# Performance work log

Hardware: AMD Instinct MI355X
Metric: run time of the kernel (lower is better)

Reference implementation:

```python
import jax, jax.numpy as jnp
import numpy as np

B, N, D_IN, D_H, D_OUT = 2, 512, 128, 128, 128


def _mlp2(x, W1, b1, W2, b2):
    # Linear -> SiLU -> Linear
    h = jax.nn.silu(x @ W1 + b1)
    return h @ W2 + b2


def _safe_norm(d2):
    # norm with zero (not NaN) gradient at 0, matching torch.norm's subgradient
    pos = d2 > 0
    return jnp.where(pos, jnp.sqrt(jnp.where(pos, d2, 1.0)), 0.0)


def setup_inputs() -> dict:
    key = jax.random.key(0)
    ks = jax.random.split(key, 16)

    def lin(k, fan_in, fan_out):
        bound = 1.0 / np.sqrt(fan_in)
        kw, kb = jax.random.split(k)
        W = jax.random.uniform(kw, (fan_in, fan_out), jnp.float32, -bound, bound)
        b = jax.random.uniform(kb, (fan_out,), jnp.float32, -bound, bound)
        return W, b

    Ws1, bs1 = lin(ks[0], D_IN, D_H)
    Ws2, bs2 = lin(ks[1], D_H, D_OUT)
    Wv1, bv1 = lin(ks[2], D_IN, D_H)
    Wv2, bv2 = lin(ks[3], D_H, D_OUT)
    Wa1, ba1 = lin(ks[4], D_IN + 3, D_H)
    Wa2, ba2 = lin(ks[5], D_H, 1)

    node_features = jax.random.normal(ks[6], (B, N, D_IN), jnp.float32)
    coordinates = jax.random.normal(ks[7], (B, N, 3), jnp.float32)
    edge_mask = jax.random.randint(ks[8], (B, N, N), 0, 2, jnp.int32)

    return dict(node_features=node_features, coordinates=coordinates, edge_mask=edge_mask,
                Ws1=Ws1, bs1=bs1, Ws2=Ws2, bs2=bs2,
                Wv1=Wv1, bv1=bv1, Wv2=Wv2, bv2=bv2,
                Wa1=Wa1, ba1=ba1, Wa2=Wa2, ba2=ba2)


def reference(node_features, coordinates, edge_mask,
              Ws1, bs1, Ws2, bs2, Wv1, bv1, Wv2, bv2, Wa1, ba1, Wa2, ba2):
    num_atoms = node_features.shape[1]

    # pairwise geometry: diff[b,i,j,:] = x_i - x_j
    diff = coordinates[:, :, None, :] - coordinates[:, None, :, :]  # [B,N,N,3]
    d2 = jnp.sum(diff * diff, axis=-1)
    distances = _safe_norm(d2)  # [B,N,N]

    # per-node scalar branch
    scalar_features = _mlp2(node_features, Ws1, bs1, Ws2, bs2)  # [B,N,D_OUT]

    # radial features + broadcast node features -> attention MLP
    dist_features = jnp.stack(
        [distances, 1.0 / (distances + 1e-6), jnp.exp(-distances)], axis=-1)  # [B,N,N,3]
    nf_exp = jnp.broadcast_to(node_features[:, :, None, :],
                              node_features.shape[:2] + (num_atoms, node_features.shape[-1]))
    attention_input = jnp.concatenate([nf_exp, dist_features], axis=-1)  # [B,N,N,D_IN+3]
    attn_logits = _mlp2(attention_input, Wa1, ba1, Wa2, ba2)[..., 0]  # [B,N,N]

    attn_logits = jnp.where(edge_mask != 0, attn_logits, -jnp.inf)
    attention_weights = jax.nn.softmax(attn_logits, axis=-1)  # [B,N,N]

    # direction-weighted aggregation
    vector_aggregated = jnp.einsum('bijc,bij->bic', diff, attention_weights)  # [B,N,3]

    vector_features = _mlp2(node_features, Wv1, bv1, Wv2, bv2)  # [B,N,D_OUT]
    vector_out = vector_aggregated * vector_features[..., :3]  # [B,N,3]

    return scalar_features, vector_out
```

## Files before the change

### kernel.cpp

```cpp
#include <hip/hip_runtime.h>
#include <math.h>

#define NB 2
#define NN 512
#define DD 128
#define LOG2E 1.4426950408889634f

typedef unsigned long long ull;

__device__ __forceinline__ float exp2_hw(float x) {
    float r; asm("v_exp_f32 %0, %1" : "=v"(r) : "v"(x)); return r;
}
__device__ __forceinline__ float silu_f(float x) {
    float e = exp2_hw(-LOG2E * x);
    return x * __builtin_amdgcn_rcpf(1.0f + e);
}

__global__ __launch_bounds__(256) void k_all(
    const float* __restrict__ nf,
    const float* __restrict__ coords,
    const int*   __restrict__ mask,
    const float* __restrict__ Ws1, const float* __restrict__ bs1,
    const float* __restrict__ Ws2, const float* __restrict__ bs2,
    const float* __restrict__ Wv1, const float* __restrict__ bv1,
    const float* __restrict__ Wv2, const float* __restrict__ bv2,
    const float* __restrict__ Wa1, const float* __restrict__ ba1,
    const float* __restrict__ Wa2, const float* __restrict__ ba2p,
    float* __restrict__ scalar_out,
    float* __restrict__ vec_out)
{
    __shared__ float  s_nf[DD];
    __shared__ float  s_part[3][256];
    __shared__ float  s_hs[DD];
    __shared__ float  s_hv[DD];
    __shared__ float4 s_pk[DD];
    __shared__ float  s_am[DD];
    __shared__ short  s_act[NN];
    __shared__ int    s_cnt8[8], s_off8[8], s_nactS;
    __shared__ float  s_red[4], s_red2[4][4];

    const int row  = blockIdx.x;
    const int b    = row >> 9;
    const int tid  = threadIdx.x;
    const int lane = tid & 63;
    const int wid  = tid >> 6;
    const int c    = tid & 127;
    const int h    = tid >> 7;

    if (tid < DD) s_nf[tid] = nf[row * DD + tid];
    __syncthreads();

    {
        float ps = 0.f, pv = 0.f, pa = 0.f;
        const int k0 = h * 64;
        #pragma unroll 8
        for (int kk = 0; kk < 64; ++kk) {
            int k   = k0 + kk;
            float x = s_nf[k];
            ps = fmaf(x, Ws1[k * DD + c], ps);
            pv = fmaf(x, Wv1[k * DD + c], pv);
            pa = fmaf(x, Wa1[k * DD + c], pa);
        }
        s_part[0][tid] = ps;
        s_part[1][tid] = pv;
        s_part[2][tid] = pa;
    }
    const int* mrow = mask + (size_t)row * NN;
    const bool m0 = (mrow[tid]       != 0);
    const bool m1 = (mrow[tid + 256] != 0);
    const ull  bal0 = __ballot(m0);
    const ull  bal1 = __ballot(m1);
    if (lane == 0) {
        s_cnt8[wid]     = __popcll(bal0);
        s_cnt8[4 + wid] = __popcll(bal1);
    }
    __syncthreads();

    if (tid < DD) {
        s_hs[tid] = silu_f(s_part[0][tid] + s_part[0][128 + tid] + bs1[tid]);
        s_hv[tid] = silu_f(s_part[1][tid] + s_part[1][128 + tid] + bv1[tid]);
        float base = s_part[2][tid] + s_part[2][128 + tid] + ba1[tid];
        float4 p;
        p.x = -LOG2E * base;
        p.y = -LOG2E * Wa1[128 * DD + tid];
        p.z = -LOG2E * Wa1[129 * DD + tid];
        p.w = -LOG2E * Wa1[130 * DD + tid];
        s_pk[tid] = p;
        s_am[tid] = -Wa2[tid];
    }
    if (tid == 0) {
        int acc = 0;
        #pragma unroll
        for (int q = 0; q < 8; ++q) { s_off8[q] = acc; acc += s_cnt8[q]; }
        s_nactS = acc;
    }
    __syncthreads();

    {
        float pb = 0.f;
        const int k0 = h * 64;
        #pragma unroll 8
        for (int kk = 0; kk < 64; ++kk) {
            int k = k0 + kk;
            pb = fmaf(s_hs[k], Ws2[k * DD + c], pb);
        }
        s_part[0][tid] = pb;
    }
    if (tid >= 128 && tid < 224) {
        int idx = tid - 128;
        int col = idx >> 5;
        int kq  = idx & 31;
        float vp = 0.f;
        #pragma unroll
        for (int u = 0; u < 4; ++u) {
            int k = 4 * kq + u;
            vp = fmaf(s_hv[k], Wv2[k * DD + col], vp);
        }
        s_part[1][tid] = vp;
    }
    {
        const ull lmask = (1ull << lane) - 1ull;
        if (m0) s_act[s_off8[wid]     + __popcll(bal0 & lmask)] = (short)tid;
        if (m1) s_act[s_off8[4 + wid] + __popcll(bal1 & lmask)] = (short)(tid + 256);
    }
    __syncthreads();

    if (tid < DD) {
        scalar_out[row * DD + tid] = s_part[0][tid] + s_part[0][128 + tid] + bs2[tid];
    }
    float vf_col = 0.f;
    if (tid < 3) {
        float v = bv2[tid];
        const float* pp = &s_part[1][128 + tid * 32];
        for (int r = 0; r < 32; ++r) v += pp[r];
        vf_col = v;
    }
    const int nact = s_nactS;

    const float ba2l = ba2p[0] * LOG2E;
    const float xi0 = coords[row * 3 + 0];
    const float xi1 = coords[row * 3 + 1];
    const float xi2 = coords[row * 3 + 2];
    const float* cb = coords + (size_t)b * NN * 3;
    const float4* A4 = (const float4*)s_am;

    float lg0 = 0.f, dx0 = 0.f, dy0 = 0.f, dz0 = 0.f;
    float lg1 = 0.f, dx1 = 0.f, dy1 = 0.f, dz1 = 0.f;
    const bool act0 = (tid < nact);
    const bool act1 = (tid + 256 < nact);

    if (act0) {
        int j = (int)s_act[tid];
        dx0 = xi0 - cb[j * 3 + 0];
        dy0 = xi1 - cb[j * 3 + 1];
        dz0 = xi2 - cb[j * 3 + 2];
        float d2 = fmaf(dx0, dx0, fmaf(dy0, dy0, dz0 * dz0));
        float d  = sqrtf(d2);
        float f1 = d;
        float x  = d + 1e-6f;
        float rc = __builtin_amdgcn_rcpf(x);
        float f2 = rc * fmaf(-x, rc, 2.0f);
        float f3 = exp2_hw(-LOG2E * d);
        float acc = ba2l;
        for (int t4 = 0; t4 < DD / 4; ++t4) {
            float4 A = A4[t4];
            { float4 P = s_pk[4*t4+0]; float pre = fmaf(f3,P.w,fmaf(f2,P.z,fmaf(f1,P.y,P.x)));
              float e = exp2_hw(pre); float r = __builtin_amdgcn_rcpf(1.0f+e);
              acc = fmaf(pre*A.x, r, acc); }
            { float4 P = s_pk[4*t4+1]; float pre = fmaf(f3,P.w,fmaf(f2,P.z,fmaf(f1,P.y,P.x)));
              float e = exp2_hw(pre); float r = __builtin_amdgcn_rcpf(1.0f+e);
              acc = fmaf(pre*A.y, r, acc); }
            { float4 P = s_pk[4*t4+2]; float pre = fmaf(f3,P.w,fmaf(f2,P.z,fmaf(f1,P.y,P.x)));
              float e = exp2_hw(pre); float r = __builtin_amdgcn_rcpf(1.0f+e);
              acc = fmaf(pre*A.z, r, acc); }
            { float4 P = s_pk[4*t4+3]; float pre = fmaf(f3,P.w,fmaf(f2,P.z,fmaf(f1,P.y,P.x)));
              float e = exp2_hw(pre); float r = __builtin_amdgcn_rcpf(1.0f+e);
              acc = fmaf(pre*A.w, r, acc); }
        }
        lg0 = acc;
    }
    if (act1) {
        int j = (int)s_act[tid + 256];
        dx1 = xi0 - cb[j * 3 + 0];
        dy1 = xi1 - cb[j * 3 + 1];
        dz1 = xi2 - cb[j * 3 + 2];
        float d2 = fmaf(dx1, dx1, fmaf(dy1, dy1, dz1 * dz1));
        float d  = sqrtf(d2);
        float f1 = d;
        float x  = d + 1e-6f;
        float rc = __builtin_amdgcn_rcpf(x);
        float f2 = rc * fmaf(-x, rc, 2.0f);
        float f3 = exp2_hw(-LOG2E * d);
        float acc = ba2l;
        for (int t4 = 0; t4 < DD / 4; ++t4) {
            float4 A = A4[t4];
            { float4 P = s_pk[4*t4+0]; float pre = fmaf(f3,P.w,fmaf(f2,P.z,fmaf(f1,P.y,P.x)));
              float e = exp2_hw(pre); float r = __builtin_amdgcn_rcpf(1.0f+e);
              acc = fmaf(pre*A.x, r, acc); }
            { float4 P = s_pk[4*t4+1]; float pre = fmaf(f3,P.w,fmaf(f2,P.z,fmaf(f1,P.y,P.x)));
              float e = exp2_hw(pre); float r = __builtin_amdgcn_rcpf(1.0f+e);
              acc = fmaf(pre*A.y, r, acc); }
            { float4 P = s_pk[4*t4+2]; float pre = fmaf(f3,P.w,fmaf(f2,P.z,fmaf(f1,P.y,P.x)));
              float e = exp2_hw(pre); float r = __builtin_amdgcn_rcpf(1.0f+e);
              acc = fmaf(pre*A.z, r, acc); }
            { float4 P = s_pk[4*t4+3]; float pre = fmaf(f3,P.w,fmaf(f2,P.z,fmaf(f1,P.y,P.x)));
              float e = exp2_hw(pre); float r = __builtin_amdgcn_rcpf(1.0f+e);
              acc = fmaf(pre*A.w, r, acc); }
        }
        lg1 = acc;
    }

    float mloc = -__builtin_inff();
    if (act0) mloc = lg0;
    if (act1) mloc = fmaxf(mloc, lg1);
    #pragma unroll
    for (int ofs = 32; ofs >= 1; ofs >>= 1) mloc = fmaxf(mloc, __shfl_xor(mloc, ofs));
    if (lane == 0) s_red[wid] = mloc;
    __syncthreads();
    const float mx = fmaxf(fmaxf(s_red[0], s_red[1]), fmaxf(s_red[2], s_red[3]));

    float es = 0.f, wx = 0.f, wy = 0.f, wz = 0.f;
    if (act0) {
        float e = exp2_hw(lg0 - mx);
        es += e; wx = fmaf(e, dx0, wx); wy = fmaf(e, dy0, wy); wz = fmaf(e, dz0, wz);
    }
    if (act1) {
        float e = exp2_hw(lg1 - mx);
        es += e; wx = fmaf(e, dx1, wx); wy = fmaf(e, dy1, wy); wz = fmaf(e, dz1, wz);
    }
    #pragma unroll
    for (int ofs = 32; ofs >= 1; ofs >>= 1) {
        es += __shfl_xor(es, ofs);
        wx += __shfl_xor(wx, ofs);
        wy += __shfl_xor(wy, ofs);
        wz += __shfl_xor(wz, ofs);
    }
    if (lane == 0) {
        s_red2[wid][0] = es; s_red2[wid][1] = wx;
        s_red2[wid][2] = wy; s_red2[wid][3] = wz;
    }
    __syncthreads();

    if (tid < 3) {
        float tot = s_red2[0][0] + s_red2[1][0] + s_red2[2][0] + s_red2[3][0];
        float num = s_red2[0][1+tid] + s_red2[1][1+tid] + s_red2[2][1+tid] + s_red2[3][1+tid];
        vec_out[row * 3 + tid] = (num / tot) * vf_col;
    }
}

extern "C" void kernel_launch(void* const* d_in, const int* in_sizes, int n_in,
                              void* d_out, int out_size, void* d_ws, size_t ws_size,
                              hipStream_t stream) {
    const float* nf     = (const float*)d_in[0];
    const float* coords = (const float*)d_in[1];
    const int*   mask   = (const int*)  d_in[2];
    const float* Ws1 = (const float*)d_in[3];  const float* bs1 = (const float*)d_in[4];
    const float* Ws2 = (const float*)d_in[5];  const float* bs2 = (const float*)d_in[6];
    const float* Wv1 = (const float*)d_in[7];  const float* bv1 = (const float*)d_in[8];
    const float* Wv2 = (const float*)d_in[9];  const float* bv2 = (const float*)d_in[10];
    const float* Wa1 = (const float*)d_in[11]; const float* ba1 = (const float*)d_in[12];
    const float* Wa2 = (const float*)d_in[13]; const float* ba2 = (const float*)d_in[14];

    float* scalar_out = (float*)d_out;
    float* vec_out    = (float*)d_out + NB * NN * DD;

    hipLaunchKernelGGL(k_all, dim3(NB * NN), dim3(256), 0, stream,
                       nf, coords, mask,
                       Ws1, bs1, Ws2, bs2, Wv1, bv1, Wv2, bv2,
                       Wa1, ba1, Wa2, ba2,
                       scalar_out, vec_out);
}
```

Before: 28.49 us.

## Overlap attention logit loop with second-layer GEMV and merge per-edge loops

Moves the attention-logit computation ahead of the barrier so it runs alongside the second-layer matvecs. It also fuses the two per-edge loops into one loop that shares the LDS loads of the packed weights, and makes the second slot wave-uniform so only partially active waves compute it. The first-layer and second-layer matvecs now read node features as float4, and the active-count prefix scan is moved earlier. The risks are extra register pressure from keeping two edge states live at once, and idle lanes in partially active waves doing wasted work.

Result: faster. 27.83 us (-2.3%).

```diff
diff --git a/kernel.cpp b/kernel.cpp
--- a/kernel.cpp
+++ b/kernel.cpp
@@ -15,6 +15,12 @@
     float e = exp2_hw(-LOG2E * x);
     return x * __builtin_amdgcn_rcpf(1.0f + e);
 }
+
+#define UPD(P, Ae, ff1, ff2, ff3, accv)                                       \
+    { float pre = fmaf(ff3, P.w, fmaf(ff2, P.z, fmaf(ff1, P.y, P.x)));        \
+      float e   = exp2_hw(pre);                                               \
+      float rc  = __builtin_amdgcn_rcpf(1.0f + e);                            \
+      accv      = fmaf(pre * Ae, rc, accv); }
 
 __global__ __launch_bounds__(256) void k_all(
     const float* __restrict__ nf,
@@ -29,12 +35,12 @@
     float* __restrict__ scalar_out,
     float* __restrict__ vec_out)
 {
-    __shared__ float  s_nf[DD];
+    __shared__ __align__(16) float s_nf[DD];
+    __shared__ __align__(16) float s_hs[DD];
+    __shared__ __align__(16) float s_hv[DD];
+    __shared__ __align__(16) float s_am[DD];
     __shared__ float  s_part[3][256];
-    __shared__ float  s_hs[DD];
-    __shared__ float  s_hv[DD];
     __shared__ float4 s_pk[DD];
-    __shared__ float  s_am[DD];
     __shared__ short  s_act[NN];
     __shared__ int    s_cnt8[8], s_off8[8], s_nactS;
     __shared__ float  s_red[4], s_red2[4][4];
@@ -48,23 +54,6 @@
     const int h    = tid >> 7;
 
     if (tid < DD) s_nf[tid] = nf[row * DD + tid];
-    __syncthreads();
-
-    {
-        float ps = 0.f, pv = 0.f, pa = 0.f;
-        const int k0 = h * 64;
-        #pragma unroll 8
-        for (int kk = 0; kk < 64; ++kk) {
-            int k   = k0 + kk;
-            float x = s_nf[k];
-            ps = fmaf(x, Ws1[k * DD + c], ps);
-            pv = fmaf(x, Wv1[k * DD + c], pv);
-            pa = fmaf(x, Wa1[k * DD + c], pa);
-        }
-        s_part[0][tid] = ps;
-        s_part[1][tid] = pv;
-        s_part[2][tid] = pa;
-    }
     const int* mrow = mask + (size_t)row * NN;
     const bool m0 = (mrow[tid]       != 0);
     const bool m1 = (mrow[tid + 256] != 0);
@@ -73,6 +62,39 @@
     if (lane == 0) {
         s_cnt8[wid]     = __popcll(bal0);
         s_cnt8[4 + wid] = __popcll(bal1);
+    }
+    __syncthreads();
+
+    if (tid == 0) {
+        int a = 0;
+        #pragma unroll
+        for (int q = 0; q < 8; ++q) { s_off8[q] = a; a += s_cnt8[q]; }
+        s_nactS = a;
+    }
+    {
+        float ps = 0.f, pv = 0.f, pa = 0.f;
+        const float4* nf4 = (const float4*)s_nf;
+        const int kq0 = h * 16;
+        #pragma unroll 4
+        for (int kk = 0; kk < 16; ++kk) {
+            float4 x = nf4[kq0 + kk];
+            const int k = (kq0 + kk) * 4;
+            ps = fmaf(x.x, Ws1[(k+0)*DD + c], ps);
+            ps = fmaf(x.y, Ws1[(k+1)*DD + c], ps);
+            ps = fmaf(x.z, Ws1[(k+2)*DD + c], ps);
+            ps = fmaf(x.w, Ws1[(k+3)*DD + c], ps);
+            pv = fmaf(x.x, Wv1[(k+0)*DD + c], pv);
+            pv = fmaf(x.y, Wv1[(k+1)*DD + c], pv);
+            pv = fmaf(x.z, Wv1[(k+2)*DD + c], pv);
+            pv = fmaf(x.w, Wv1[(k+3)*DD + c], pv);
+            pa = fmaf(x.x, Wa1[(k+0)*DD + c], pa);
+            pa = fmaf(x.y, Wa1[(k+1)*DD + c], pa);
+            pa = fmaf(x.z, Wa1[(k+2)*DD + c], pa);
+            pa = fmaf(x.w, Wa1[(k+3)*DD + c], pa);
+        }
+        s_part[0][tid] = ps;
+        s_part[1][tid] = pv;
+        s_part[2][tid] = pa;
     }
     __syncthreads();
 
@@ -88,40 +110,100 @@
         s_pk[tid] = p;
         s_am[tid] = -Wa2[tid];
     }
-    if (tid == 0) {
-        int acc = 0;
-        #pragma unroll
-        for (int q = 0; q < 8; ++q) { s_off8[q] = acc; acc += s_cnt8[q]; }
-        s_nactS = acc;
+    {
+        const ull lm = (1ull << lane) - 1ull;
+        if (m0) s_act[s_off8[wid]     + __popcll(bal0 & lm)] = (short)tid;
+        if (m1) s_act[s_off8[4 + wid] + __popcll(bal1 & lm)] = (short)(tid + 256);
     }
     __syncthreads();
 
     {
         float pb = 0.f;
-        const int k0 = h * 64;
-        #pragma unroll 8
-        for (int kk = 0; kk < 64; ++kk) {
-            int k = k0 + kk;
-            pb = fmaf(s_hs[k], Ws2[k * DD + c], pb);
+        const float4* hs4 = (const float4*)s_hs;
+        const int kq0 = h * 16;
+        #pragma unroll 4
+        for (int kk = 0; kk < 16; ++kk) {
+            float4 x = hs4[kq0 + kk];
+            const int k = (kq0 + kk) * 4;
+            pb = fmaf(x.x, Ws2[(k+0)*DD + c], pb);
+            pb = fmaf(x.y, Ws2[(k+1)*DD + c], pb);
+            pb = fmaf(x.z, Ws2[(k+2)*DD + c], pb);
+            pb = fmaf(x.w, Ws2[(k+3)*DD + c], pb);
         }
         s_part[0][tid] = pb;
     }
     if (tid >= 128 && tid < 224) {
-        int idx = tid - 128;
-        int col = idx >> 5;
-        int kq  = idx & 31;
+        const int idx = tid - 128;
+        const int col = idx >> 5;
+        const int kq  = idx & 31;
         float vp = 0.f;
         #pragma unroll
         for (int u = 0; u < 4; ++u) {
-            int k = 4 * kq + u;
+            const int k = 4 * kq + u;
             vp = fmaf(s_hv[k], Wv2[k * DD + col], vp);
         }
         s_part[1][tid] = vp;
     }
-    {
-        const ull lmask = (1ull << lane) - 1ull;
-        if (m0) s_act[s_off8[wid]     + __popcll(bal0 & lmask)] = (short)tid;
-        if (m1) s_act[s_off8[4 + wid] + __popcll(bal1 & lmask)] = (short)(tid + 256);
+
+    const int nact = __builtin_amdgcn_readfirstlane(s_nactS);
+    const bool act0 = (tid < nact);
+    const bool act1 = (tid + 256 < nact);
+    const bool w_has1 = ((tid & ~63) + 256) < nact;
+
+    const float ba2l = ba2p[0] * LOG2E;
+    const float xi0 = coords[row * 3 + 0];
+    const float xi1 = coords[row * 3 + 1];
+    const float xi2 = coords[row * 3 + 2];
+    const float* cb = coords + (size_t)b * NN * 3;
+
+    float dx0 = 0.f, dy0 = 0.f, dz0 = 0.f, f1_0 = 0.f, f2_0 = 0.f, f3_0 = 0.f;
+    float dx1 = 0.f, dy1 = 0.f, dz1 = 0.f, f1_1 = 0.f, f2_1 = 0.f, f3_1 = 0.f;
+    float acc0 = ba2l, acc1 = ba2l;
+
+    {
+        const int j = ((int)s_act[act0 ? tid : 0]) & (NN - 1);
+        dx0 = xi0 - cb[j * 3 + 0];
+        dy0 = xi1 - cb[j * 3 + 1];
+        dz0 = xi2 - cb[j * 3 + 2];
+        float d2 = fmaf(dx0, dx0, fmaf(dy0, dy0, dz0 * dz0));
+        float d  = sqrtf(d2);
+        f1_0 = d;
+        float x  = d + 1e-6f;
+        float rc = __builtin_amdgcn_rcpf(x);
+        f2_0 = rc * fmaf(-x, rc, 2.0f);
+        f3_0 = exp2_hw(-LOG2E * d);
+    }
+    if (w_has1) {
+        const int j = ((int)s_act[act1 ? tid + 256 : 0]) & (NN - 1);
+        dx1 = xi0 - cb[j * 3 + 0];
+        dy1 = xi1 - cb[j * 3 + 1];
+        dz1 = xi2 - cb[j * 3 + 2];
+        float d2 = fmaf(dx1, dx1, fmaf(dy1, dy1, dz1 * dz1));
+        float d  = sqrtf(d2);
+        f1_1 = d;
+        float x  = d + 1e-6f;
+        float rc = __builtin_amdgcn_rcpf(x);
+        f2_1 = rc * fmaf(-x, rc, 2.0f);
+        f3_1 = exp2_hw(-LOG2E * d);
+    }
+
+    const float4* A4 = (const float4*)s_am;
+    for (int t4 = 0; t4 < DD / 4; ++t4) {
+        float4 A  = A4[t4];
+        float4 P0 = s_pk[4 * t4 + 0];
+        float4 P1 = s_pk[4 * t4 + 1];
+        float4 P2 = s_pk[4 * t4 + 2];
+        float4 P3 = s_pk[4 * t4 + 3];
+        UPD(P0, A.x, f1_0, f2_0, f3_0, acc0);
+        UPD(P1, A.y, f1_0, f2_0, f3_0, acc0);
+        UPD(P2, A.z, f1_0, f2_0, f3_0, acc0);
+        UPD(P3, A.w, f1_0, f2_0, f3_0, acc0);
+        if (w_has1) {
+            UPD(P0, A.x, f1_1, f2_1, f3_1, acc1);
+            UPD(P1, A.y, f1_1, f2_1, f3_1, acc1);
+            UPD(P2, A.z, f1_1, f2_1, f3_1, acc1);
+            UPD(P3, A.w, f1_1, f2_1, f3_1, acc1);
+        }
     }
     __syncthreads();
 
@@ -135,84 +217,10 @@
         for (int r = 0; r < 32; ++r) v += pp[r];
         vf_col = v;
     }
-    const int nact = s_nactS;
-
-    const float ba2l = ba2p[0] * LOG2E;
-    const float xi0 = coords[row * 3 + 0];
-    const float xi1 = coords[row * 3 + 1];
-    const float xi2 = coords[row * 3 + 2];
-    const float* cb = coords + (size_t)b * NN * 3;
-    const float4* A4 = (const float4*)s_am;
-
-    float lg0 = 0.f, dx0 = 0.f, dy0 = 0.f, dz0 = 0.f;
-    float lg1 = 0.f, dx1 = 0.f, dy1 = 0.f, dz1 = 0.f;
-    const bool act0 = (tid < nact);
-    const bool act1 = (tid + 256 < nact);
-
-    if (act0) {
-        int j = (int)s_act[tid];
-        dx0 = xi0 - cb[j * 3 + 0];
-        dy0 = xi1 - cb[j * 3 + 1];
-        dz0 = xi2 - cb[j * 3 + 2];
-        float d2 = fmaf(dx0, dx0, fmaf(dy0, dy0, dz0 * dz0));
-        float d  = sqrtf(d2);
-        float f1 = d;
-        float x  = d + 1e-6f;
-        float rc = __builtin_amdgcn_rcpf(x);
-        float f2 = rc * fmaf(-x, rc, 2.0f);
-        float f3 = exp2_hw(-LOG2E * d);
-        float acc = ba2l;
-        for (int t4 = 0; t4 < DD / 4; ++t4) {
-            float4 A = A4[t4];
-            { float4 P = s_pk[4*t4+0]; float pre = fmaf(f3,P.w,fmaf(f2,P.z,fmaf(f1,P.y,P.x)));
-              float e = exp2_hw(pre); float r = __builtin_amdgcn_rcpf(1.0f+e);
-              acc = fmaf(pre*A.x, r, acc); }
-            { float4 P = s_pk[4*t4+1]; float pre = fmaf(f3,P.w,fmaf(f2,P.z,fmaf(f1,P.y,P.x)));
-              float e = exp2_hw(pre); float r = __builtin_amdgcn_rcpf(1.0f+e);
-              acc = fmaf(pre*A.y, r, acc); }
-            { float4 P = s_pk[4*t4+2]; float pre = fmaf(f3,P.w,fmaf(f2,P.z,fmaf(f1,P.y,P.x)));
-              float e = exp2_hw(pre); float r = __builtin_amdgcn_rcpf(1.0f+e);
-              acc = fmaf(pre*A.z, r, acc); }
-            { float4 P = s_pk[4*t4+3]; float pre = fmaf(f3,P.w,fmaf(f2,P.z,fmaf(f1,P.y,P.x)));
-              float e = exp2_hw(pre); float r = __builtin_amdgcn_rcpf(1.0f+e);
-              acc = fmaf(pre*A.w, r, acc); }
-        }
-        lg0 = acc;
-    }
-    if (act1) {
-        int j = (int)s_act[tid + 256];
-        dx1 = xi0 - cb[j * 3 + 0];
-        dy1 = xi1 - cb[j * 3 + 1];
-        dz1 = xi2 - cb[j * 3 + 2];
-        float d2 = fmaf(dx1, dx1, fmaf(dy1, dy1, dz1 * dz1));
-        float d  = sqrtf(d2);
-        float f1 = d;
-        float x  = d + 1e-6f;
-        float rc = __builtin_amdgcn_rcpf(x);
-        float f2 = rc * fmaf(-x, rc, 2.0f);
-        float f3 = exp2_hw(-LOG2E * d);
-        float acc = ba2l;
-        for (int t4 = 0; t4 < DD / 4; ++t4) {
-            float4 A = A4[t4];
-            { float4 P = s_pk[4*t4+0]; float pre = fmaf(f3,P.w,fmaf(f2,P.z,fmaf(f1,P.y,P.x)));
-              float e = exp2_hw(pre); float r = __builtin_amdgcn_rcpf(1.0f+e);
-              acc = fmaf(pre*A.x, r, acc); }
-            { float4 P = s_pk[4*t4+1]; float pre = fmaf(f3,P.w,fmaf(f2,P.z,fmaf(f1,P.y,P.x)));
-              float e = exp2_hw(pre); float r = __builtin_amdgcn_rcpf(1.0f+e);
-              acc = fmaf(pre*A.y, r, acc); }
-            { float4 P = s_pk[4*t4+2]; float pre = fmaf(f3,P.w,fmaf(f2,P.z,fmaf(f1,P.y,P.x)));
-              float e = exp2_hw(pre); float r = __builtin_amdgcn_rcpf(1.0f+e);
-              acc = fmaf(pre*A.z, r, acc); }
-            { float4 P = s_pk[4*t4+3]; float pre = fmaf(f3,P.w,fmaf(f2,P.z,fmaf(f1,P.y,P.x)));
-              float e = exp2_hw(pre); float r = __builtin_amdgcn_rcpf(1.0f+e);
-              acc = fmaf(pre*A.w, r, acc); }
-        }
-        lg1 = acc;
-    }
 
     float mloc = -__builtin_inff();
-    if (act0) mloc = lg0;
-    if (act1) mloc = fmaxf(mloc, lg1);
+    if (act0) mloc = acc0;
+    if (act1) mloc = fmaxf(mloc, acc1);
     #pragma unroll
     for (int ofs = 32; ofs >= 1; ofs >>= 1) mloc = fmaxf(mloc, __shfl_xor(mloc, ofs));
     if (lane == 0) s_red[wid] = mloc;
@@ -221,11 +229,11 @@
 
     float es = 0.f, wx = 0.f, wy = 0.f, wz = 0.f;
     if (act0) {
-        float e = exp2_hw(lg0 - mx);
+        float e = exp2_hw(acc0 - mx);
         es += e; wx = fmaf(e, dx0, wx); wy = fmaf(e, dy0, wy); wz = fmaf(e, dz0, wz);
     }
-    if (act1) {
-        float e = exp2_hw(lg1 - mx);
+    if (w_has1 && act1) {
+        float e = exp2_hw(acc1 - mx);
         es += e; wx = fmaf(e, dx1, wx); wy = fmaf(e, dy1, wy); wz = fmaf(e, dz1, wz);
     }
     #pragma unroll
```
